# Kernel tuning notes

Measured on AMD Instinct MI355X. Metric: run time of the kernel, lower is better.

## Reference

```python
import jax, jax.numpy as jnp
import numpy as np

N = 4096   # node_each_graph == in_feats (adjacency-row node features)
H = 512    # n_hidden
C = 2      # n_classes
E = 65536  # edges (avg degree 16)
NL = 5     # n_layers -> 4 GINConv layers
NR = NL - 2  # stacked hidden GIN layers (layers 1..3)


def _bn(x, g, b, m, v):
    # BatchNorm1d in eval mode (running stats), eps=1e-5
    return (x - m) * jax.lax.rsqrt(v + 1e-5) * g + b


def setup_inputs():
    key = jax.random.key(0)
    ks = iter(jax.random.split(key, 16))
    nk = lambda: next(ks)
    s = 0.02
    f32 = jnp.float32
    d = {}
    d["feat"] = jax.random.normal(nk(), (N, N), f32)
    d["edge_src"] = jax.random.randint(nk(), (E,), 0, N)
    d["edge_dst"] = jax.random.randint(nk(), (E,), 0, N)
    # GIN layer 0: MLP is Linear(N,H)-BN-ReLU-Linear(H,H); ApplyNodeFunc BN; outer BN
    d["eps0"] = jnp.zeros((), f32)
    d["W0a"] = jax.random.normal(nk(), (N, H), f32) * s
    d["b0a"] = jnp.zeros((H,), f32)
    d["W0b"] = jax.random.normal(nk(), (H, H), f32) * s
    d["b0b"] = jnp.zeros((H,), f32)
    for nm in ["bn0a", "bnA0", "bnO0"]:
        d[nm + "_g"] = jnp.ones((H,), f32); d[nm + "_b"] = jnp.zeros((H,), f32)
        d[nm + "_m"] = jnp.zeros((H,), f32); d[nm + "_v"] = jnp.ones((H,), f32)
    # GIN layers 1..NL-2 stacked (H -> H)
    d["epsR"] = jnp.zeros((NR,), f32)
    d["WRa"] = jax.random.normal(nk(), (NR, H, H), f32) * s
    d["bRa"] = jnp.zeros((NR, H), f32)
    d["WRb"] = jax.random.normal(nk(), (NR, H, H), f32) * s
    d["bRb"] = jnp.zeros((NR, H), f32)
    for nm in ["bnRa", "bnAR", "bnOR"]:
        d[nm + "_g"] = jnp.ones((NR, H), f32); d[nm + "_b"] = jnp.zeros((NR, H), f32)
        d[nm + "_m"] = jnp.zeros((NR, H), f32); d[nm + "_v"] = jnp.ones((NR, H), f32)
    # per-hidden-rep readout linears (batch_size = 1)
    d["Wp0"] = jax.random.normal(nk(), (N * N, C), f32) * 0.001
    d["bp0"] = jnp.zeros((C,), f32)
    d["WpR"] = jax.random.normal(nk(), (NL - 1, N * H, C), f32) * 0.001
    d["bpR"] = jnp.zeros((NL - 1, C), f32)
    return d


def _gin(h, src, dst, eps, Wa, ba, bna, Wb, bb, bnA, bnO):
    # GINConv sum-aggregation: (1+eps)*h + sum over in-neighbors
    agg = jax.ops.segment_sum(h[src], dst, num_segments=N)
    x = (1.0 + eps) * h + agg
    # MLP (num_layers=2): Linear -> BN -> ReLU -> Linear
    x = jax.nn.relu(_bn(x @ Wa + ba, *bna))
    x = x @ Wb + bb
    # ApplyNodeFunc: BN -> ReLU
    x = jax.nn.relu(_bn(x, *bnA))
    # Model-level BN -> ReLU
    x = jax.nn.relu(_bn(x, *bnO))
    return x


def reference(feat, edge_src, edge_dst, eps0, W0a, b0a, W0b, b0b,
              bn0a_g, bn0a_b, bn0a_m, bn0a_v, bnA0_g, bnA0_b, bnA0_m, bnA0_v,
              bnO0_g, bnO0_b, bnO0_m, bnO0_v,
              epsR, WRa, bRa, WRb, bRb,
              bnRa_g, bnRa_b, bnRa_m, bnRa_v, bnAR_g, bnAR_b, bnAR_m, bnAR_v,
              bnOR_g, bnOR_b, bnOR_m, bnOR_v, Wp0, bp0, WpR, bpR):
    h = _gin(feat, edge_src, edge_dst, eps0, W0a, b0a,
             (bn0a_g, bn0a_b, bn0a_m, bn0a_v), W0b, b0b,
             (bnA0_g, bnA0_b, bnA0_m, bnA0_v), (bnO0_g, bnO0_b, bnO0_m, bnO0_v))
    hs = [h]
    for i in range(NR):  # small fixed layer loop
        h = _gin(h, edge_src, edge_dst, epsR[i], WRa[i], bRa[i],
                 (bnRa_g[i], bnRa_b[i], bnRa_m[i], bnRa_v[i]), WRb[i], bRb[i],
                 (bnAR_g[i], bnAR_b[i], bnAR_m[i], bnAR_v[i]),
                 (bnOR_g[i], bnOR_b[i], bnOR_m[i], bnOR_v[i]))
        hs.append(h)
    # jumping-knowledge readout over hidden_rep (eval: dropout = identity)
    score = feat.reshape(1, -1) @ Wp0 + bp0
    for i, hi in enumerate(hs):
        score = score + hi.reshape(1, -1) @ WpR[i] + bpR[i]
    return score
```

## Files before the change

### kernel.cpp

```cpp
#include <hip/hip_runtime.h>
#include <cstdint>
#include <cstddef>

typedef __attribute__((ext_vector_type(8))) short short8;
typedef __attribute__((ext_vector_type(4))) float f32x4;
typedef __attribute__((ext_vector_type(4))) float f4;
typedef __attribute__((ext_vector_type(2))) float f2;
typedef __attribute__((ext_vector_type(4))) unsigned short us4;

#define NN 4096
#define HH 512
#define EE 65536

#define GLOAD(gp, lp) __builtin_amdgcn_global_load_lds( \
    (const __attribute__((address_space(1))) void*)(gp), \
    (__attribute__((address_space(3))) void*)(lp), 16, 0, 0)

__device__ __forceinline__ unsigned short f2bf(float x) {
    union { float f; unsigned u; } un; un.f = x;
    unsigned r = un.u + 0x7fffu + ((un.u >> 16) & 1u);
    return (unsigned short)(r >> 16);
}
__device__ __forceinline__ float b2f(unsigned short v) {
    union { unsigned u; float f; } un; un.u = ((unsigned)v) << 16; return un.f;
}

__global__ __launch_bounds__(1024) void k_histscan(const int* __restrict__ edst,
                                                   int* __restrict__ starts) {
    __shared__ int cnt[NN];
    __shared__ int wtot[16], woff[16];
    const int t = threadIdx.x;
    for (int i = t; i < NN; i += 1024) cnt[i] = 0;
    __syncthreads();
    for (int i = t; i < EE; i += 1024) atomicAdd(&cnt[edst[i]], 1);
    __syncthreads();
    const int b = t * 4;
    const int c0 = cnt[b], c1 = cnt[b + 1], c2 = cnt[b + 2], c3 = cnt[b + 3];
    const int s = c0 + c1 + c2 + c3;
    const int lane = t & 63, wv = t >> 6;
    int inc = s;
    for (int d = 1; d < 64; d <<= 1) {
        int v = __shfl_up(inc, d);
        if (lane >= d) inc += v;
    }
    if (lane == 63) wtot[wv] = inc;
    __syncthreads();
    if (t == 0) {
        int a = 0;
        for (int i = 0; i < 16; ++i) { woff[i] = a; a += wtot[i]; }
        starts[NN] = a;
    }
    __syncthreads();
    int run = woff[wv] + inc - s;
    starts[b] = run; run += c0;
    starts[b + 1] = run; run += c1;
    starts[b + 2] = run; run += c2;
    starts[b + 3] = run;
}

__global__ void k_scatter(const int* __restrict__ src, const int* __restrict__ dst,
                          const int* __restrict__ starts, int* __restrict__ cursor,
                          int* __restrict__ sorted) {
    int e = blockIdx.x * 256 + threadIdx.x;
    if (e < EE) {
        int d = dst[e];
        int p = starts[d] + atomicAdd(&cursor[d], 1);
        sorted[p] = src[e];
    }
}

__global__ void k_binsort(const int* __restrict__ starts, int* __restrict__ a) {
    int d = blockIdx.x * 256 + threadIdx.x;
    if (d < NN) {
        int s = starts[d], e = starts[d + 1];
        for (int i = s + 1; i < e; ++i) {
            int v = a[i]; int j = i - 1;
            while (j >= s && a[j] > v) { a[j + 1] = a[j]; --j; }
            a[j + 1] = v;
        }
    }
}

__global__ __launch_bounds__(256) void k_cvtdot0(const float* __restrict__ feat,
                                                 const float* __restrict__ w,
                                                 unsigned short* __restrict__ featb,
                                                 float* __restrict__ part) {
    __shared__ f4 fs[1024];
    __shared__ float s0[256], s1[256];
    const int t = threadIdx.x;
    const long B0 = (long)blockIdx.x * 1024;
    const f4* ff = (const f4*)feat;
    const f4* ww = (const f4*)w;
    f4 v[4];
#pragma unroll
    for (int k = 0; k < 4; ++k)
        v[k] = __builtin_nontemporal_load(ff + B0 + k * 256 + t);
#pragma unroll
    for (int k = 0; k < 4; ++k) {
        fs[k * 256 + t] = v[k];
        us4 o;
        o.x = f2bf(v[k].x); o.y = f2bf(v[k].y); o.z = f2bf(v[k].z); o.w = f2bf(v[k].w);
        ((us4*)featb)[B0 + k * 256 + t] = o;
    }
    f4 wv[8];
#pragma unroll
    for (int k = 0; k < 8; ++k)
        wv[k] = __builtin_nontemporal_load(ww + 2 * B0 + k * 256 + t);
    __syncthreads();
    float a0 = 0.f, a1 = 0.f;
#pragma unroll
    for (int k = 0; k < 8; ++k) {
        const int q = k * 256 + t;
        f2 fp = *(const f2*)((const char*)fs + (size_t)q * 8);
        a0 += fp.x * wv[k].x + fp.y * wv[k].z;
        a1 += fp.x * wv[k].y + fp.y * wv[k].w;
    }
    s0[t] = a0; s1[t] = a1;
    __syncthreads();
    for (int s = 128; s > 0; s >>= 1) {
        if (t < s) { s0[t] += s0[t + s]; s1[t] += s1[t + s]; }
        __syncthreads();
    }
    if (t == 0) { part[2 * blockIdx.x] = s0[0]; part[2 * blockIdx.x + 1] = s1[0]; }
}

__global__ __launch_bounds__(256) void k_transcvt8(const float* __restrict__ W0a,
                                                   const float* __restrict__ W0b,
                                                   const float* __restrict__ WRa,
                                                   const float* __restrict__ WRb,
                                                   unsigned short* __restrict__ w0at,
                                                   unsigned short* __restrict__ wt) {
    __shared__ float tile[32][33];
    const int z = blockIdx.z;
    const float* W;
    unsigned short* Wt;
    int K;
    if (z == 7) {
        W = W0a; Wt = w0at; K = NN;
    } else {
        if (blockIdx.x >= 16 || blockIdx.y >= 16) return;
        W = (z == 0) ? W0b : (z < 4) ? WRa + (size_t)(z - 1) * HH * HH
                                     : WRb + (size_t)(z - 4) * HH * HH;
        Wt = wt + (size_t)z * HH * HH; K = HH;
    }
    const int k0 = blockIdx.x * 32, n0 = blockIdx.y * 32;
    const int tx = threadIdx.x & 31, ty = threadIdx.x >> 5;
    for (int r = ty; r < 32; r += 8)
        tile[r][tx] = W[(size_t)(k0 + r) * HH + n0 + tx];
    __syncthreads();
    for (int r = ty; r < 32; r += 8)
        Wt[(size_t)(n0 + r) * K + k0 + tx] = f2bf(tile[tx][r]);
}

__global__ __launch_bounds__(256) void k_gemm0(
    const unsigned short* __restrict__ A, const unsigned short* __restrict__ Bt,
    int M, int N, int K, float* __restrict__ outf)
{
    __shared__ alignas(16) unsigned short As[2][128 * 32];
    __shared__ alignas(16) unsigned short Bs[2][128 * 32];
    const int t = threadIdx.x;
    const int lane = t & 63, w = t >> 6;
    const int wr = w >> 1, wc = w & 1;
    const int l15 = lane & 15, l4 = lane >> 4;
    const int m0 = blockIdx.x * 128, n0 = blockIdx.y * 128;

    f32x4 acc[4][4];
#pragma unroll
    for (int i = 0; i < 4; ++i)
#pragma unroll
        for (int j = 0; j < 4; ++j) acc[i][j] = (f32x4){0.f, 0.f, 0.f, 0.f};

    const int Kc = K / gridDim.z;
    const int kbase = blockIdx.z * Kc;
    const unsigned short* ga0 = A + (size_t)m0 * K + kbase + (size_t)(t >> 2) * K + (t & 3) * 8;
    const unsigned short* ga1 = ga0 + (size_t)64 * K;
    const unsigned short* gb0 = Bt + (size_t)n0 * K + kbase + (size_t)(t >> 2) * K + (t & 3) * 8;
    const unsigned short* gb1 = gb0 + (size_t)64 * K;

    auto stage = [&](int kt, int buf) {
        const int ko = kt * 32;
        GLOAD(ga0 + ko, &As[buf][t * 8]);
        GLOAD(ga1 + ko, &As[buf][(t + 256) * 8]);
        GLOAD(gb0 + ko, &Bs[buf][t * 8]);
        GLOAD(gb1 + ko, &Bs[buf][(t + 256) * 8]);
    };

    const int nk = Kc >> 5;
    stage(0, 0);
    __syncthreads();
    for (int kt = 0; kt < nk; ++kt) {
        const int cur = kt & 1;
        if (kt + 1 < nk) stage(kt + 1, cur ^ 1);
        short8 aF[4], bF[4];
#pragma unroll
        for (int i = 0; i < 4; ++i)
            aF[i] = *(const short8*)(&As[cur][(wr * 64 + i * 16 + l15) * 32 + 8 * l4]);
#pragma unroll
        for (int j = 0; j < 4; ++j)
            bF[j] = *(const short8*)(&Bs[cur][(wc * 64 + j * 16 + l15) * 32 + 8 * l4]);
#pragma unroll
        for (int i = 0; i < 4; ++i)
#pragma unroll
            for (int j = 0; j < 4; ++j)
                acc[i][j] = __builtin_amdgcn_mfma_f32_16x16x32_bf16(aF[i], bF[j], acc[i][j], 0, 0, 0);
        __syncthreads();
    }

    const int mrow = m0 + wr * 64;
    float* op = outf + (size_t)blockIdx.z * M * N;
#pragma unroll
    for (int j = 0; j < 4; ++j) {
        const int cg = n0 + wc * 64 + j * 16 + l15;
#pragma unroll
        for (int i = 0; i < 4; ++i)
#pragma unroll
            for (int r = 0; r < 4; ++r)
                op[(size_t)(mrow + i * 16 + l4 * 4 + r) * N + cg] = acc[i][j][r];
    }
}

template<int EPI, bool DOT>
__global__ __launch_bounds__(512) void k_gemmH(
    const unsigned short* __restrict__ A, const unsigned short* __restrict__ Bt,
    const float* __restrict__ bias,
    const float* __restrict__ g1p, const float* __restrict__ b1p,
    const float* __restrict__ m1p, const float* __restrict__ v1p,
    const float* __restrict__ g2p, const float* __restrict__ b2p,
    const float* __restrict__ m2p, const float* __restrict__ v2p,
    unsigned short* __restrict__ outb,
    const float* __restrict__ wq, float* __restrict__ part, int slotbase)
{
    constexpr int K = HH, N = HH;
    __shared__ alignas(16) unsigned short As[2][128 * 32];
    __shared__ alignas(16) unsigned short Bs[2][64 * 32];
    const int t = threadIdx.x;
    const int lane = t & 63, w = t >> 6;
    const int wr = w >> 1, wc = w & 1;
    const int l15 = lane & 15, l4 = lane >> 4;
    const int m0 = blockIdx.x * 128, n0 = blockIdx.y * 64;

    f32x4 acc[2][2];
#pragma unroll
    for (int i = 0; i < 2; ++i)
#pragma unroll
        for (int j = 0; j < 2; ++j) acc[i][j] = (f32x4){0.f, 0.f, 0.f, 0.f};

    const unsigned short* ga = A + (size_t)m0 * K + (size_t)(t >> 2) * K + (t & 3) * 8;
    const unsigned short* gb = Bt + (size_t)n0 * K + (size_t)(t >> 2) * K + (t & 3) * 8;

    auto stage = [&](int kt, int buf) {
        const int ko = kt * 32;
        GLOAD(ga + ko, &As[buf][t * 8]);
        if (t < 256) GLOAD(gb + ko, &Bs[buf][t * 8]);
    };

    const int nk = K >> 5;
    stage(0, 0);
    __syncthreads();
    for (int kt = 0; kt < nk; ++kt) {
        const int cur = kt & 1;
        if (kt + 1 < nk) stage(kt + 1, cur ^ 1);
        short8 aF[2], bF[2];
#pragma unroll
        for (int i = 0; i < 2; ++i)
            aF[i] = *(const short8*)(&As[cur][(wr * 32 + i * 16 + l15) * 32 + 8 * l4]);
#pragma unroll
        for (int j = 0; j < 2; ++j)
            bF[j] = *(const short8*)(&Bs[cur][(wc * 32 + j * 16 + l15) * 32 + 8 * l4]);
#pragma unroll
        for (int i = 0; i < 2; ++i)
#pragma unroll
            for (int j = 0; j < 2; ++j)
                acc[i][j] = __builtin_amdgcn_mfma_f32_16x16x32_bf16(aF[i], bF[j], acc[i][j], 0, 0, 0);
        __syncthreads();
    }

    const int mrow = m0 + wr * 32;
    float d0 = 0.f, d1 = 0.f;
#pragma unroll
    for (int j = 0; j < 2; ++j) {
        const int cg = n0 + wc * 32 + j * 16 + l15;
        const float bi = bias[cg];
        const float sc1 = rsqrtf(v1p[cg] + 1e-5f) * g1p[cg];
        const float sh1 = b1p[cg] - m1p[cg] * sc1;
        float sc2 = 1.f, sh2 = 0.f;
        if (EPI == 3) {
            sc2 = rsqrtf(v2p[cg] + 1e-5f) * g2p[cg];
            sh2 = b2p[cg] - m2p[cg] * sc2;
        }
#pragma unroll
        for (int i = 0; i < 2; ++i) {
#pragma unroll
            for (int r = 0; r < 4; ++r) {
                const int rg = mrow + i * 16 + l4 * 4 + r;
                float x = acc[i][j][r];
                x = fmaxf((x + bi) * sc1 + sh1, 0.f);
                if (EPI == 3) x = fmaxf(x * sc2 + sh2, 0.f);
                outb[(size_t)rg * N + cg] = f2bf(x);
                if constexpr (DOT) {
                    float2 wvv = ((const float2*)wq)[(size_t)rg * N + cg];
                    d0 += x * wvv.x; d1 += x * wvv.y;
                }
            }
        }
    }
    if constexpr (DOT) {
        __shared__ float r0[512], r1[512];
        r0[t] = d0; r1[t] = d1;
        __syncthreads();
        for (int s = 256; s > 0; s >>= 1) {
            if (t < s) { r0[t] += r0[t + s]; r1[t] += r1[t + s]; }
            __syncthreads();
        }
        if (t == 0) {
            const int slot = slotbase + blockIdx.y * gridDim.x + blockIdx.x;
            part[2 * slot] = r0[0]; part[2 * slot + 1] = r1[0];
        }
    }
}

__global__ __launch_bounds__(256) void k_red4b(const float* __restrict__ p,
                                               unsigned short* __restrict__ G0b) {
    const long S = (long)NN * HH / 4;
    long i = blockIdx.x * 256L + threadIdx.x;
    float4 a = ((const float4*)p)[i];
    float4 b = ((const float4*)p)[i + S];
    float4 c = ((const float4*)p)[i + 2 * S];
    float4 d = ((const float4*)p)[i + 3 * S];
    us4 o;
    o.x = f2bf((a.x + b.x) + (c.x + d.x));
    o.y = f2bf((a.y + b.y) + (c.y + d.y));
    o.z = f2bf((a.z + b.z) + (c.z + d.z));
    o.w = f2bf((a.w + b.w) + (c.w + d.w));
    ((us4*)G0b)[i] = o;
}

__global__ __launch_bounds__(128) void k_agg0(
    const unsigned short* __restrict__ G0, const int* __restrict__ starts,
    const int* __restrict__ sorted, const float* __restrict__ epsp,
    const float* __restrict__ bias,
    const float* __restrict__ bg, const float* __restrict__ bb,
    const float* __restrict__ bm, const float* __restrict__ bv,
    unsigned short* __restrict__ outb)
{
    const int d = blockIdx.x, t = threadIdx.x;
    const float ep = 1.0f + epsp[0];
    ushort4 ow = ((const ushort4*)(G0 + (size_t)d * HH))[t];
    float sx = 0.f, sy = 0.f, sz = 0.f, sw = 0.f;
    const int e0 = starts[d], e1 = starts[d + 1];
    int i = e0;
    for (; i + 4 <= e1; i += 4) {
        int q0 = sorted[i], q1 = sorted[i + 1], q2 = sorted[i + 2], q3 = sorted[i + 3];
        ushort4 x0 = ((const ushort4*)(G0 + (size_t)q0 * HH))[t];
        ushort4 x1 = ((const ushort4*)(G0 + (size_t)q1 * HH))[t];
        ushort4 x2 = ((const ushort4*)(G0 + (size_t)q2 * HH))[t];
        ushort4 x3 = ((const ushort4*)(G0 + (size_t)q3 * HH))[t];
        sx += (b2f(x0.x) + b2f(x1.x)) + (b2f(x2.x) + b2f(x3.x));
        sy += (b2f(x0.y) + b2f(x1.y)) + (b2f(x2.y) + b2f(x3.y));
        sz += (b2f(x0.z) + b2f(x1.z)) + (b2f(x2.z) + b2f(x3.z));
        sw += (b2f(x0.w) + b2f(x1.w)) + (b2f(x2.w) + b2f(x3.w));
    }
    for (; i < e1; ++i) {
        ushort4 x = ((const ushort4*)(G0 + (size_t)sorted[i] * HH))[t];
        sx += b2f(x.x); sy += b2f(x.y); sz += b2f(x.z); sw += b2f(x.w);
    }
    float4 bi = ((const float4*)bias)[t];
    float4 g4 = ((const float4*)bg)[t];
    float4 b4 = ((const float4*)bb)[t];
    float4 m4 = ((const float4*)bm)[t];
    float4 v4 = ((const float4*)bv)[t];
    float x0 = ep * b2f(ow.x) + sx + bi.x;
    float x1 = ep * b2f(ow.y) + sy + bi.y;
    float x2 = ep * b2f(ow.z) + sz + bi.z;
    float x3 = ep * b2f(ow.w) + sw + bi.w;
    x0 = fmaxf((x0 - m4.x) * rsqrtf(v4.x + 1e-5f) * g4.x + b4.x, 0.f);
    x1 = fmaxf((x1 - m4.y) * rsqrtf(v4.y + 1e-5f) * g4.y + b4.y, 0.f);
    x2 = fmaxf((x2 - m4.z) * rsqrtf(v4.z + 1e-5f) * g4.z + b4.z, 0.f);
    x3 = fmaxf((x3 - m4.w) * rsqrtf(v4.w + 1e-5f) * g4.w + b4.w, 0.f);
    ushort4 o; o.x = f2bf(x0); o.y = f2bf(x1); o.z = f2bf(x2); o.w = f2bf(x3);
    ((ushort4*)(outb + (size_t)d * HH))[t] = o;
}

__global__ __launch_bounds__(128) void k_aggL(
    const unsigned short* __restrict__ hsrc, const int* __restrict__ starts,
    const int* __restrict__ sorted, const float* __restrict__ epsp,
    unsigned short* __restrict__ outb)
{
    const int d = blockIdx.x, t = threadIdx.x;
    const float ep = 1.0f + epsp[0];
    ushort4 ow = ((const ushort4*)(hsrc + (size_t)d * HH))[t];
    float sx = 0.f, sy = 0.f, sz = 0.f, sw = 0.f;
    const int e0 = starts[d], e1 = starts[d + 1];
    int i = e0;
    for (; i + 4 <= e1; i += 4) {
        int q0 = sorted[i], q1 = sorted[i + 1], q2 = sorted[i + 2], q3 = sorted[i + 3];
        ushort4 x0 = ((const ushort4*)(hsrc + (size_t)q0 * HH))[t];
        ushort4 x1 = ((const ushort4*)(hsrc + (size_t)q1 * HH))[t];
        ushort4 x2 = ((const ushort4*)(hsrc + (size_t)q2 * HH))[t];
        ushort4 x3 = ((const ushort4*)(hsrc + (size_t)q3 * HH))[t];
        sx += (b2f(x0.x) + b2f(x1.x)) + (b2f(x2.x) + b2f(x3.x));
        sy += (b2f(x0.y) + b2f(x1.y)) + (b2f(x2.y) + b2f(x3.y));
        sz += (b2f(x0.z) + b2f(x1.z)) + (b2f(x2.z) + b2f(x3.z));
        sw += (b2f(x0.w) + b2f(x1.w)) + (b2f(x2.w) + b2f(x3.w));
    }
    for (; i < e1; ++i) {
        ushort4 x = ((const ushort4*)(hsrc + (size_t)sorted[i] * HH))[t];
        sx += b2f(x.x); sy += b2f(x.y); sz += b2f(x.z); sw += b2f(x.w);
    }
    ushort4 o;
    o.x = f2bf(ep * b2f(ow.x) + sx);
    o.y = f2bf(ep * b2f(ow.y) + sy);
    o.z = f2bf(ep * b2f(ow.z) + sz);
    o.w = f2bf(ep * b2f(ow.w) + sw);
    ((ushort4*)(outb + (size_t)d * HH))[t] = o;
}

__global__ __launch_bounds__(256) void k_final(const float* __restrict__ part, int nslot,
                                               const float* __restrict__ bp0, const float* __restrict__ bpR,
                                               float* __restrict__ out) {
    __shared__ float s0[256], s1[256];
    int t = threadIdx.x;
    float a0 = 0.f, a1 = 0.f;
    for (int i = t; i < nslot; i += 256) { a0 += part[2 * i]; a1 += part[2 * i + 1]; }
    s0[t] = a0; s1[t] = a1;
    __syncthreads();
    for (int s = 128; s > 0; s >>= 1) {
        if (t < s) { s0[t] += s0[t + s]; s1[t] += s1[t + s]; }
        __syncthreads();
    }
    if (t == 0) {
        out[0] = s0[0] + bp0[0] + bpR[0] + bpR[2] + bpR[4] + bpR[6];
        out[1] = s1[0] + bp0[1] + bpR[1] + bpR[3] + bpR[5] + bpR[7];
    }
}

extern "C" void kernel_launch(void* const* d_in, const int* in_sizes, int n_in,
                              void* d_out, int out_size, void* d_ws, size_t ws_size,
                              hipStream_t stream)
{
    const float* feat = (const float*)d_in[0];
    const int*   esrc = (const int*)d_in[1];
    const int*   edst = (const int*)d_in[2];
    const float* eps0 = (const float*)d_in[3];
    const float* W0a  = (const float*)d_in[4];
    const float* b0a  = (const float*)d_in[5];
    const float* W0b  = (const float*)d_in[6];
    const float* b0b  = (const float*)d_in[7];
    const float* bn0a_g = (const float*)d_in[8];
    const float* bn0a_b = (const float*)d_in[9];
    const float* bn0a_m = (const float*)d_in[10];
    const float* bn0a_v = (const float*)d_in[11];
    const float* bnA0_g = (const float*)d_in[12];
    const float* bnA0_b = (const float*)d_in[13];
    const float* bnA0_m = (const float*)d_in[14];
    const float* bnA0_v = (const float*)d_in[15];
    const float* bnO0_g = (const float*)d_in[16];
    const float* bnO0_b = (const float*)d_in[17];
    const float* bnO0_m = (const float*)d_in[18];
    const float* bnO0_v = (const float*)d_in[19];
    const float* epsR = (const float*)d_in[20];
    const float* WRa  = (const float*)d_in[21];
    const float* bRa  = (const float*)d_in[22];
    const float* WRb  = (const float*)d_in[23];
    const float* bRb  = (const float*)d_in[24];
    const float* bnRa_g = (const float*)d_in[25];
    const float* bnRa_b = (const float*)d_in[26];
    const float* bnRa_m = (const float*)d_in[27];
    const float* bnRa_v = (const float*)d_in[28];
    const float* bnAR_g = (const float*)d_in[29];
    const float* bnAR_b = (const float*)d_in[30];
    const float* bnAR_m = (const float*)d_in[31];
    const float* bnAR_v = (const float*)d_in[32];
    const float* bnOR_g = (const float*)d_in[33];
    const float* bnOR_b = (const float*)d_in[34];
    const float* bnOR_m = (const float*)d_in[35];
    const float* bnOR_v = (const float*)d_in[36];
    const float* Wp0 = (const float*)d_in[37];
    const float* bp0 = (const float*)d_in[38];
    const float* WpR = (const float*)d_in[39];
    const float* bpR = (const float*)d_in[40];
    float* out = (float*)d_out;

    char* ws = (char*)d_ws;
    const size_t MB = 1024 * 1024;
    int*   starts = (int*)(ws + 0x10000);
    int*   cursor = (int*)(ws + 0x20000);
    int*   sorted = (int*)(ws + 0x30000);
    float* part   = (float*)(ws + 0x70000);
    unsigned short* featb = (unsigned short*)(ws + 1 * MB);
    unsigned short* w0at  = (unsigned short*)(ws + 33 * MB);
    unsigned short* wt    = (unsigned short*)(ws + 37 * MB);
    unsigned short* G0b   = (unsigned short*)(ws + 41 * MB);
    unsigned short* xb = (unsigned short*)(ws + 49 * MB);
    unsigned short* yb = (unsigned short*)(ws + 53 * MB);
    unsigned short* hb = (unsigned short*)(ws + 57 * MB);
    float* pbuf = (float*)(ws + 57 * MB);

    hipMemsetAsync(cursor, 0, NN * sizeof(int), stream);
    k_histscan<<<1, 1024, 0, stream>>>(edst, starts);
    k_scatter<<<EE / 256, 256, 0, stream>>>(esrc, edst, starts, cursor, sorted);
    k_binsort<<<NN / 256, 256, 0, stream>>>(starts, sorted);

    k_cvtdot0<<<4096, 256, 0, stream>>>(feat, Wp0, featb, part);
    k_transcvt8<<<dim3(NN / 32, HH / 32, 8), 256, 0, stream>>>(W0a, W0b, WRa, WRb, w0at, wt);

    k_gemm0<<<dim3(32, 4, 4), 256, 0, stream>>>(featb, w0at, NN, HH, NN, pbuf);
    k_red4b<<<2048, 256, 0, stream>>>(pbuf, G0b);
    k_agg0<<<NN, 128, 0, stream>>>(G0b, starts, sorted, eps0, b0a,
                                   bn0a_g, bn0a_b, bn0a_m, bn0a_v, xb);
    k_gemmH<3, true><<<dim3(32, 8), 512, 0, stream>>>(xb, wt,
        b0b, bnA0_g, bnA0_b, bnA0_m, bnA0_v, bnO0_g, bnO0_b, bnO0_m, bnO0_v,
        hb, WpR, part, 4096);

    for (int i = 0; i < 3; ++i) {
        const unsigned short* hp = hb + (size_t)i * NN * HH;
        unsigned short* hn = hb + (size_t)(i + 1) * NN * HH;
        k_aggL<<<NN, 128, 0, stream>>>(hp, starts, sorted, epsR + i, xb);
        k_gemmH<1, false><<<dim3(32, 8), 512, 0, stream>>>(xb, wt + (size_t)(1 + i) * HH * HH,
            bRa + (size_t)i * HH,
            bnRa_g + (size_t)i * HH, bnRa_b + (size_t)i * HH, bnRa_m + (size_t)i * HH, bnRa_v + (size_t)i * HH,
            nullptr, nullptr, nullptr, nullptr,
            yb, nullptr, nullptr, 0);
        k_gemmH<3, true><<<dim3(32, 8), 512, 0, stream>>>(yb, wt + (size_t)(4 + i) * HH * HH,
            bRb + (size_t)i * HH,
            bnAR_g + (size_t)i * HH, bnAR_b + (size_t)i * HH, bnAR_m + (size_t)i * HH, bnAR_v + (size_t)i * HH,
            bnOR_g + (size_t)i * HH, bnOR_b + (size_t)i * HH, bnOR_m + (size_t)i * HH, bnOR_v + (size_t)i * HH,
            hn, WpR + (size_t)(i + 1) * NN * HH * 2, part, 4096 + (i + 1) * 256);
    }

    k_final<<<1, 256, 0, stream>>>(part, 4096 + 4 * 256, bp0, bpR, out);
}
```

Before: 299.6 us.

## Fuse GIN layer kernels into a persistent megakernel with grid barriers

```diff
diff --git a/kernel.cpp b/kernel.cpp
--- a/kernel.cpp
+++ b/kernel.cpp
@@ -11,6 +11,7 @@
 #define NN 4096
 #define HH 512
 #define EE 65536
+#define NBLK 256
 
 #define GLOAD(gp, lp) __builtin_amdgcn_global_load_lds( \
     (const __attribute__((address_space(1))) void*)(gp), \
@@ -23,6 +24,18 @@
 }
 __device__ __forceinline__ float b2f(unsigned short v) {
     union { unsigned u; float f; } un; un.u = ((unsigned)v) << 16; return un.f;
+}
+
+__device__ __forceinline__ void gbar(int* cnt, int target) {
+    __syncthreads();
+    if (threadIdx.x == 0) {
+        __threadfence();
+        __hip_atomic_fetch_add(cnt, 1, __ATOMIC_RELEASE, __HIP_MEMORY_SCOPE_AGENT);
+        while (__hip_atomic_load(cnt, __ATOMIC_ACQUIRE, __HIP_MEMORY_SCOPE_AGENT) < target)
+            __builtin_amdgcn_s_sleep(1);
+        __threadfence();
+    }
+    __syncthreads();
 }
 
 __global__ __launch_bounds__(1024) void k_histscan(const int* __restrict__ edst,
@@ -81,197 +94,155 @@
     }
 }
 
-__global__ __launch_bounds__(256) void k_cvtdot0(const float* __restrict__ feat,
-                                                 const float* __restrict__ w,
-                                                 unsigned short* __restrict__ featb,
-                                                 float* __restrict__ part) {
+__global__ __launch_bounds__(256) void k_prep(const float* __restrict__ feat,
+                                              const float* __restrict__ Wp0,
+                                              unsigned short* __restrict__ featb,
+                                              float* __restrict__ part,
+                                              const float* __restrict__ W0a,
+                                              const float* __restrict__ W0b,
+                                              const float* __restrict__ WRa,
+                                              const float* __restrict__ WRb,
+                                              unsigned short* __restrict__ w0at,
+                                              unsigned short* __restrict__ wt) {
     __shared__ f4 fs[1024];
     __shared__ float s0[256], s1[256];
+    __shared__ float tile[32][33];
     const int t = threadIdx.x;
-    const long B0 = (long)blockIdx.x * 1024;
-    const f4* ff = (const f4*)feat;
-    const f4* ww = (const f4*)w;
-    f4 v[4];
-#pragma unroll
-    for (int k = 0; k < 4; ++k)
-        v[k] = __builtin_nontemporal_load(ff + B0 + k * 256 + t);
-#pragma unroll
-    for (int k = 0; k < 4; ++k) {
-        fs[k * 256 + t] = v[k];
-        us4 o;
-        o.x = f2bf(v[k].x); o.y = f2bf(v[k].y); o.z = f2bf(v[k].z); o.w = f2bf(v[k].w);
-        ((us4*)featb)[B0 + k * 256 + t] = o;
-    }
-    f4 wv[8];
-#pragma unroll
-    for (int k = 0; k < 8; ++k)
-        wv[k] = __builtin_nontemporal_load(ww + 2 * B0 + k * 256 + t);
-    __syncthreads();
-    float a0 = 0.f, a1 = 0.f;
-#pragma unroll
-    for (int k = 0; k < 8; ++k) {
-        const int q = k * 256 + t;
-        f2 fp = *(const f2*)((const char*)fs + (size_t)q * 8);
-        a0 += fp.x * wv[k].x + fp.y * wv[k].z;
-        a1 += fp.x * wv[k].y + fp.y * wv[k].w;
-    }
-    s0[t] = a0; s1[t] = a1;
-    __syncthreads();
-    for (int s = 128; s > 0; s >>= 1) {
-        if (t < s) { s0[t] += s0[t + s]; s1[t] += s1[t + s]; }
-        __syncthreads();
-    }
-    if (t == 0) { part[2 * blockIdx.x] = s0[0]; part[2 * blockIdx.x + 1] = s1[0]; }
-}
-
-__global__ __launch_bounds__(256) void k_transcvt8(const float* __restrict__ W0a,
-                                                   const float* __restrict__ W0b,
-                                                   const float* __restrict__ WRa,
-                                                   const float* __restrict__ WRb,
-                                                   unsigned short* __restrict__ w0at,
-                                                   unsigned short* __restrict__ wt) {
-    __shared__ float tile[32][33];
-    const int z = blockIdx.z;
-    const float* W;
-    unsigned short* Wt;
-    int K;
-    if (z == 7) {
-        W = W0a; Wt = w0at; K = NN;
+    const int bid = blockIdx.x;
+    if (bid < 4096) {
+        const long B0 = (long)bid * 1024;
+        const f4* ff = (const f4*)feat;
+        const f4* ww = (const f4*)Wp0;
+        f4 v[4];
+#pragma unroll
+        for (int k = 0; k < 4; ++k)
+            v[k] = __builtin_nontemporal_load(ff + B0 + k * 256 + t);
+#pragma unroll
+        for (int k = 0; k < 4; ++k) {
+            fs[k * 256 + t] = v[k];
+            us4 o;
+            o.x = f2bf(v[k].x); o.y = f2bf(v[k].y); o.z = f2bf(v[k].z); o.w = f2bf(v[k].w);
+            __builtin_nontemporal_store(o, (us4*)featb + B0 + k * 256 + t);
+        }
+        f4 wv[8];
+#pragma unroll
+        for (int k = 0; k < 8; ++k)
+            wv[k] = __builtin_nontemporal_load(ww + 2 * B0 + k * 256 + t);
+        __syncthreads();
+        float a0 = 0.f, a1 = 0.f;
+#pragma unroll
+        for (int k = 0; k < 8; ++k) {
+            const int q = k * 256 + t;
+            f2 fp = *(const f2*)((const char*)fs + (size_t)q * 8);
+            a0 += fp.x * wv[k].x + fp.y * wv[k].z;
+            a1 += fp.x * wv[k].y + fp.y * wv[k].w;
+        }
+        s0[t] = a0; s1[t] = a1;
+        __syncthreads();
+        for (int s = 128; s > 0; s >>= 1) {
+            if (t < s) { s0[t] += s0[t + s]; s1[t] += s1[t + s]; }
+            __syncthreads();
+        }
+        if (t == 0) { part[2 * bid] = s0[0]; part[2 * bid + 1] = s1[0]; }
     } else {
-        if (blockIdx.x >= 16 || blockIdx.y >= 16) return;
-        W = (z == 0) ? W0b : (z < 4) ? WRa + (size_t)(z - 1) * HH * HH
-                                     : WRb + (size_t)(z - 4) * HH * HH;
-        Wt = wt + (size_t)z * HH * HH; K = HH;
-    }
-    const int k0 = blockIdx.x * 32, n0 = blockIdx.y * 32;
-    const int tx = threadIdx.x & 31, ty = threadIdx.x >> 5;
-    for (int r = ty; r < 32; r += 8)
-        tile[r][tx] = W[(size_t)(k0 + r) * HH + n0 + tx];
-    __syncthreads();
-    for (int r = ty; r < 32; r += 8)
-        Wt[(size_t)(n0 + r) * K + k0 + tx] = f2bf(tile[tx][r]);
-}
-
-__global__ __launch_bounds__(256) void k_gemm0(
-    const unsigned short* __restrict__ A, const unsigned short* __restrict__ Bt,
-    int M, int N, int K, float* __restrict__ outf)
+        const int tix = bid - 4096;
+        const float* W; unsigned short* Wt; int K, kb, nb;
+        if (tix < 2048) {
+            W = W0a; Wt = w0at; K = NN; kb = tix >> 4; nb = tix & 15;
+        } else {
+            const int t2 = tix - 2048;
+            const int z = t2 >> 8, r = t2 & 255;
+            W = (z == 0) ? W0b : (z < 4) ? WRa + (size_t)(z - 1) * HH * HH
+                                         : WRb + (size_t)(z - 4) * HH * HH;
+            Wt = wt + (size_t)z * HH * HH; K = HH; kb = r >> 4; nb = r & 15;
+        }
+        const int k0 = kb * 32, n0 = nb * 32;
+        const int tx = t & 31, ty = t >> 5;
+        for (int r = ty; r < 32; r += 8)
+            tile[r][tx] = W[(size_t)(k0 + r) * HH + n0 + tx];
+        __syncthreads();
+        for (int r = ty; r < 32; r += 8)
+            Wt[(size_t)(n0 + r) * K + k0 + tx] = f2bf(tile[tx][r]);
+    }
+}
+
+struct MegaArgs {
+    const unsigned short *featb, *w0at, *wt;
+    unsigned short *G0b, *xb, *yb, *hb;
+    const int *starts, *sorted;
+    const float *eps0, *b0a, *bn0a_g, *bn0a_b, *bn0a_m, *bn0a_v;
+    const float *b0b, *bnA0_g, *bnA0_b, *bnA0_m, *bnA0_v;
+    const float *bnO0_g, *bnO0_b, *bnO0_m, *bnO0_v;
+    const float *epsR, *bRa, *bnRa_g, *bnRa_b, *bnRa_m, *bnRa_v;
+    const float *bRb, *bnAR_g, *bnAR_b, *bnAR_m, *bnAR_v;
+    const float *bnOR_g, *bnOR_b, *bnOR_m, *bnOR_v;
+    const float *WpR, *bp0, *bpR;
+    float *part, *out;
+    int *bar;
+};
+
+template<int EPI, bool DOT>
+__device__ __forceinline__ void gemm_phase(
+    const unsigned short* __restrict__ A, const unsigned short* __restrict__ Bt, int K,
+    const float* __restrict__ bias,
+    const float* __restrict__ g1, const float* __restrict__ b1,
+    const float* __restrict__ m1, const float* __restrict__ v1,
+    const float* __restrict__ g2, const float* __restrict__ b2,
+    const float* __restrict__ m2, const float* __restrict__ v2,
+    unsigned short* __restrict__ outb,
+    const float* __restrict__ wq, float* __restrict__ part, int slot,
+    unsigned short* As, unsigned short* Bs)
 {
-    __shared__ alignas(16) unsigned short As[2][128 * 32];
-    __shared__ alignas(16) unsigned short Bs[2][128 * 32];
+    constexpr int N = HH;
     const int t = threadIdx.x;
     const int lane = t & 63, w = t >> 6;
     const int wr = w >> 1, wc = w & 1;
     const int l15 = lane & 15, l4 = lane >> 4;
-    const int m0 = blockIdx.x * 128, n0 = blockIdx.y * 128;
-
-    f32x4 acc[4][4];
-#pragma unroll
-    for (int i = 0; i < 4; ++i)
-#pragma unroll
-        for (int j = 0; j < 4; ++j) acc[i][j] = (f32x4){0.f, 0.f, 0.f, 0.f};
-
-    const int Kc = K / gridDim.z;
-    const int kbase = blockIdx.z * Kc;
-    const unsigned short* ga0 = A + (size_t)m0 * K + kbase + (size_t)(t >> 2) * K + (t & 3) * 8;
+    const int m0 = (blockIdx.x >> 3) * 128, n0 = (blockIdx.x & 7) * 64;
+
+    f32x4 acc[2][2];
+#pragma unroll
+    for (int i = 0; i < 2; ++i)
+#pragma unroll
+        for (int j = 0; j < 2; ++j) acc[i][j] = (f32x4){0.f, 0.f, 0.f, 0.f};
+
+    const unsigned short* ga0 = A + (size_t)(m0 + (t >> 3)) * K + (t & 7) * 8;
     const unsigned short* ga1 = ga0 + (size_t)64 * K;
-    const unsigned short* gb0 = Bt + (size_t)n0 * K + kbase + (size_t)(t >> 2) * K + (t & 3) * 8;
-    const unsigned short* gb1 = gb0 + (size_t)64 * K;
+    const unsigned short* gb  = Bt + (size_t)(n0 + (t >> 3)) * K + (t & 7) * 8;
 
     auto stage = [&](int kt, int buf) {
-        const int ko = kt * 32;
-        GLOAD(ga0 + ko, &As[buf][t * 8]);
-        GLOAD(ga1 + ko, &As[buf][(t + 256) * 8]);
-        GLOAD(gb0 + ko, &Bs[buf][t * 8]);
-        GLOAD(gb1 + ko, &Bs[buf][(t + 256) * 8]);
+        const int ko = kt * 64;
+        GLOAD(ga0 + ko, As + buf * 8192 + t * 8);
+        GLOAD(ga1 + ko, As + buf * 8192 + 4096 + t * 8);
+        GLOAD(gb + ko,  Bs + buf * 4096 + t * 8);
     };
 
-    const int nk = Kc >> 5;
+    const int nk = K >> 6;
     stage(0, 0);
     __syncthreads();
     for (int kt = 0; kt < nk; ++kt) {
         const int cur = kt & 1;
         if (kt + 1 < nk) stage(kt + 1, cur ^ 1);
-        short8 aF[4], bF[4];
-#pragma unroll
-        for (int i = 0; i < 4; ++i)
-            aF[i] = *(const short8*)(&As[cur][(wr * 64 + i * 16 + l15) * 32 + 8 * l4]);
-#pragma unroll
-        for (int j = 0; j < 4; ++j)
-            bF[j] = *(const short8*)(&Bs[cur][(wc * 64 + j * 16 + l15) * 32 + 8 * l4]);
-#pragma unroll
-        for (int i = 0; i < 4; ++i)
-#pragma unroll
-            for (int j = 0; j < 4; ++j)
-                acc[i][j] = __builtin_amdgcn_mfma_f32_16x16x32_bf16(aF[i], bF[j], acc[i][j], 0, 0, 0);
-        __syncthreads();
-    }
-
-    const int mrow = m0 + wr * 64;
-    float* op = outf + (size_t)blockIdx.z * M * N;
-#pragma unroll
-    for (int j = 0; j < 4; ++j) {
-        const int cg = n0 + wc * 64 + j * 16 + l15;
-#pragma unroll
-        for (int i = 0; i < 4; ++i)
-#pragma unroll
-            for (int r = 0; r < 4; ++r)
-                op[(size_t)(mrow + i * 16 + l4 * 4 + r) * N + cg] = acc[i][j][r];
-    }
-}
-
-template<int EPI, bool DOT>
-__global__ __launch_bounds__(512) void k_gemmH(
-    const unsigned short* __restrict__ A, const unsigned short* __restrict__ Bt,
-    const float* __restrict__ bias,
-    const float* __restrict__ g1p, const float* __restrict__ b1p,
-    const float* __restrict__ m1p, const float* __restrict__ v1p,
-    const float* __restrict__ g2p, const float* __restrict__ b2p,
-    const float* __restrict__ m2p, const float* __restrict__ v2p,
-    unsigned short* __restrict__ outb,
-    const float* __restrict__ wq, float* __restrict__ part, int slotbase)
-{
-    constexpr int K = HH, N = HH;
-    __shared__ alignas(16) unsigned short As[2][128 * 32];
-    __shared__ alignas(16) unsigned short Bs[2][64 * 32];
-    const int t = threadIdx.x;
-    const int lane = t & 63, w = t >> 6;
-    const int wr = w >> 1, wc = w & 1;
-    const int l15 = lane & 15, l4 = lane >> 4;
-    const int m0 = blockIdx.x * 128, n0 = blockIdx.y * 64;
-
-    f32x4 acc[2][2];
-#pragma unroll
-    for (int i = 0; i < 2; ++i)
-#pragma unroll
-        for (int j = 0; j < 2; ++j) acc[i][j] = (f32x4){0.f, 0.f, 0.f, 0.f};
-
-    const unsigned short* ga = A + (size_t)m0 * K + (size_t)(t >> 2) * K + (t & 3) * 8;
-    const unsigned short* gb = Bt + (size_t)n0 * K + (size_t)(t >> 2) * K + (t & 3) * 8;
-
-    auto stage = [&](int kt, int buf) {
-        const int ko = kt * 32;
-        GLOAD(ga + ko, &As[buf][t * 8]);
-        if (t < 256) GLOAD(gb + ko, &Bs[buf][t * 8]);
-    };
-
-    const int nk = K >> 5;
-    stage(0, 0);
-    __syncthreads();
-    for (int kt = 0; kt < nk; ++kt) {
-        const int cur = kt & 1;
-        if (kt + 1 < nk) stage(kt + 1, cur ^ 1);
-        short8 aF[2], bF[2];
+        const unsigned short* Ac = As + cur * 8192;
+        const unsigned short* Bc = Bs + cur * 4096;
+        short8 aF[2][2], bF[2][2];
 #pragma unroll
         for (int i = 0; i < 2; ++i)
-            aF[i] = *(const short8*)(&As[cur][(wr * 32 + i * 16 + l15) * 32 + 8 * l4]);
+#pragma unroll
+            for (int ks = 0; ks < 2; ++ks)
+                aF[i][ks] = *(const short8*)(Ac + (wr * 32 + i * 16 + l15) * 64 + ks * 32 + l4 * 8);
 #pragma unroll
         for (int j = 0; j < 2; ++j)
-            bF[j] = *(const short8*)(&Bs[cur][(wc * 32 + j * 16 + l15) * 32 + 8 * l4]);
-#pragma unroll
-        for (int i = 0; i < 2; ++i)
-#pragma unroll
-            for (int j = 0; j < 2; ++j)
-                acc[i][j] = __builtin_amdgcn_mfma_f32_16x16x32_bf16(aF[i], bF[j], acc[i][j], 0, 0, 0);
+#pragma unroll
+            for (int ks = 0; ks < 2; ++ks)
+                bF[j][ks] = *(const short8*)(Bc + (wc * 32 + j * 16 + l15) * 64 + ks * 32 + l4 * 8);
+#pragma unroll
+        for (int ks = 0; ks < 2; ++ks)
+#pragma unroll
+            for (int i = 0; i < 2; ++i)
+#pragma unroll
+                for (int j = 0; j < 2; ++j)
+                    acc[i][j] = __builtin_amdgcn_mfma_f32_16x16x32_bf16(aF[i][ks], bF[j][ks], acc[i][j], 0, 0, 0);
         __syncthreads();
     }
 
@@ -280,13 +251,15 @@
 #pragma unroll
     for (int j = 0; j < 2; ++j) {
         const int cg = n0 + wc * 32 + j * 16 + l15;
-        const float bi = bias[cg];
-        const float sc1 = rsqrtf(v1p[cg] + 1e-5f) * g1p[cg];
-        const float sh1 = b1p[cg] - m1p[cg] * sc1;
-        float sc2 = 1.f, sh2 = 0.f;
+        float bi = 0.f, sc1 = 1.f, sh1 = 0.f, sc2 = 1.f, sh2 = 0.f;
+        if (EPI >= 1) {
+            bi = bias[cg];
+            sc1 = rsqrtf(v1[cg] + 1e-5f) * g1[cg];
+            sh1 = b1[cg] - m1[cg] * sc1;
+        }
         if (EPI == 3) {
-            sc2 = rsqrtf(v2p[cg] + 1e-5f) * g2p[cg];
-            sh2 = b2p[cg] - m2p[cg] * sc2;
+            sc2 = rsqrtf(v2[cg] + 1e-5f) * g2[cg];
+            sh2 = b2[cg] - m2[cg] * sc2;
         }
 #pragma unroll
         for (int i = 0; i < 2; ++i) {
@@ -294,143 +267,143 @@
             for (int r = 0; r < 4; ++r) {
                 const int rg = mrow + i * 16 + l4 * 4 + r;
                 float x = acc[i][j][r];
-                x = fmaxf((x + bi) * sc1 + sh1, 0.f);
-                if (EPI == 3) x = fmaxf(x * sc2 + sh2, 0.f);
+                if (EPI >= 1) {
+                    x = fmaxf((x + bi) * sc1 + sh1, 0.f);
+                    if (EPI == 3) x = fmaxf(x * sc2 + sh2, 0.f);
+                }
                 outb[(size_t)rg * N + cg] = f2bf(x);
                 if constexpr (DOT) {
-                    float2 wvv = ((const float2*)wq)[(size_t)rg * N + cg];
+                    f2 wvv = __builtin_nontemporal_load((const f2*)wq + (size_t)rg * N + cg);
                     d0 += x * wvv.x; d1 += x * wvv.y;
                 }
             }
         }
     }
     if constexpr (DOT) {
-        __shared__ float r0[512], r1[512];
+        float* r0 = (float*)As;
+        float* r1 = r0 + 512;
+        __syncthreads();
         r0[t] = d0; r1[t] = d1;
         __syncthreads();
         for (int s = 256; s > 0; s >>= 1) {
             if (t < s) { r0[t] += r0[t + s]; r1[t] += r1[t + s]; }
             __syncthreads();
         }
-        if (t == 0) {
-            const int slot = slotbase + blockIdx.y * gridDim.x + blockIdx.x;
-            part[2 * slot] = r0[0]; part[2 * slot + 1] = r1[0];
-        }
-    }
-}
-
-__global__ __launch_bounds__(256) void k_red4b(const float* __restrict__ p,
-                                               unsigned short* __restrict__ G0b) {
-    const long S = (long)NN * HH / 4;
-    long i = blockIdx.x * 256L + threadIdx.x;
-    float4 a = ((const float4*)p)[i];
-    float4 b = ((const float4*)p)[i + S];
-    float4 c = ((const float4*)p)[i + 2 * S];
-    float4 d = ((const float4*)p)[i + 3 * S];
-    us4 o;
-    o.x = f2bf((a.x + b.x) + (c.x + d.x));
-    o.y = f2bf((a.y + b.y) + (c.y + d.y));
-    o.z = f2bf((a.z + b.z) + (c.z + d.z));
-    o.w = f2bf((a.w + b.w) + (c.w + d.w));
-    ((us4*)G0b)[i] = o;
-}
-
-__global__ __launch_bounds__(128) void k_agg0(
-    const unsigned short* __restrict__ G0, const int* __restrict__ starts,
-    const int* __restrict__ sorted, const float* __restrict__ epsp,
+        if (t == 0) { part[2 * slot] = r0[0]; part[2 * slot + 1] = r1[0]; }
+    }
+}
+
+template<bool L0>
+__device__ __forceinline__ void agg_phase(
+    const unsigned short* __restrict__ src, unsigned short* __restrict__ dst,
+    const int* __restrict__ starts, const int* __restrict__ sorted, float ep,
     const float* __restrict__ bias,
     const float* __restrict__ bg, const float* __restrict__ bb,
-    const float* __restrict__ bm, const float* __restrict__ bv,
-    unsigned short* __restrict__ outb)
+    const float* __restrict__ bm, const float* __restrict__ bv)
 {
-    const int d = blockIdx.x, t = threadIdx.x;
-    const float ep = 1.0f + epsp[0];
-    ushort4 ow = ((const ushort4*)(G0 + (size_t)d * HH))[t];
-    float sx = 0.f, sy = 0.f, sz = 0.f, sw = 0.f;
-    const int e0 = starts[d], e1 = starts[d + 1];
-    int i = e0;
-    for (; i + 4 <= e1; i += 4) {
-        int q0 = sorted[i], q1 = sorted[i + 1], q2 = sorted[i + 2], q3 = sorted[i + 3];
-        ushort4 x0 = ((const ushort4*)(G0 + (size_t)q0 * HH))[t];
-        ushort4 x1 = ((const ushort4*)(G0 + (size_t)q1 * HH))[t];
-        ushort4 x2 = ((const ushort4*)(G0 + (size_t)q2 * HH))[t];
-        ushort4 x3 = ((const ushort4*)(G0 + (size_t)q3 * HH))[t];
-        sx += (b2f(x0.x) + b2f(x1.x)) + (b2f(x2.x) + b2f(x3.x));
-        sy += (b2f(x0.y) + b2f(x1.y)) + (b2f(x2.y) + b2f(x3.y));
-        sz += (b2f(x0.z) + b2f(x1.z)) + (b2f(x2.z) + b2f(x3.z));
-        sw += (b2f(x0.w) + b2f(x1.w)) + (b2f(x2.w) + b2f(x3.w));
-    }
-    for (; i < e1; ++i) {
-        ushort4 x = ((const ushort4*)(G0 + (size_t)sorted[i] * HH))[t];
-        sx += b2f(x.x); sy += b2f(x.y); sz += b2f(x.z); sw += b2f(x.w);
-    }
-    float4 bi = ((const float4*)bias)[t];
-    float4 g4 = ((const float4*)bg)[t];
-    float4 b4 = ((const float4*)bb)[t];
-    float4 m4 = ((const float4*)bm)[t];
-    float4 v4 = ((const float4*)bv)[t];
-    float x0 = ep * b2f(ow.x) + sx + bi.x;
-    float x1 = ep * b2f(ow.y) + sy + bi.y;
-    float x2 = ep * b2f(ow.z) + sz + bi.z;
-    float x3 = ep * b2f(ow.w) + sw + bi.w;
-    x0 = fmaxf((x0 - m4.x) * rsqrtf(v4.x + 1e-5f) * g4.x + b4.x, 0.f);
-    x1 = fmaxf((x1 - m4.y) * rsqrtf(v4.y + 1e-5f) * g4.y + b4.y, 0.f);
-    x2 = fmaxf((x2 - m4.z) * rsqrtf(v4.z + 1e-5f) * g4.z + b4.z, 0.f);
-    x3 = fmaxf((x3 - m4.w) * rsqrtf(v4.w + 1e-5f) * g4.w + b4.w, 0.f);
-    ushort4 o; o.x = f2bf(x0); o.y = f2bf(x1); o.z = f2bf(x2); o.w = f2bf(x3);
-    ((ushort4*)(outb + (size_t)d * HH))[t] = o;
-}
-
-__global__ __launch_bounds__(128) void k_aggL(
-    const unsigned short* __restrict__ hsrc, const int* __restrict__ starts,
-    const int* __restrict__ sorted, const float* __restrict__ epsp,
-    unsigned short* __restrict__ outb)
-{
-    const int d = blockIdx.x, t = threadIdx.x;
-    const float ep = 1.0f + epsp[0];
-    ushort4 ow = ((const ushort4*)(hsrc + (size_t)d * HH))[t];
-    float sx = 0.f, sy = 0.f, sz = 0.f, sw = 0.f;
-    const int e0 = starts[d], e1 = starts[d + 1];
-    int i = e0;
-    for (; i + 4 <= e1; i += 4) {
-        int q0 = sorted[i], q1 = sorted[i + 1], q2 = sorted[i + 2], q3 = sorted[i + 3];
-        ushort4 x0 = ((const ushort4*)(hsrc + (size_t)q0 * HH))[t];
-        ushort4 x1 = ((const ushort4*)(hsrc + (size_t)q1 * HH))[t];
-        ushort4 x2 = ((const ushort4*)(hsrc + (size_t)q2 * HH))[t];
-        ushort4 x3 = ((const ushort4*)(hsrc + (size_t)q3 * HH))[t];
-        sx += (b2f(x0.x) + b2f(x1.x)) + (b2f(x2.x) + b2f(x3.x));
-        sy += (b2f(x0.y) + b2f(x1.y)) + (b2f(x2.y) + b2f(x3.y));
-        sz += (b2f(x0.z) + b2f(x1.z)) + (b2f(x2.z) + b2f(x3.z));
-        sw += (b2f(x0.w) + b2f(x1.w)) + (b2f(x2.w) + b2f(x3.w));
-    }
-    for (; i < e1; ++i) {
-        ushort4 x = ((const ushort4*)(hsrc + (size_t)sorted[i] * HH))[t];
-        sx += b2f(x.x); sy += b2f(x.y); sz += b2f(x.z); sw += b2f(x.w);
-    }
-    ushort4 o;
-    o.x = f2bf(ep * b2f(ow.x) + sx);
-    o.y = f2bf(ep * b2f(ow.y) + sy);
-    o.z = f2bf(ep * b2f(ow.z) + sz);
-    o.w = f2bf(ep * b2f(ow.w) + sw);
-    ((ushort4*)(outb + (size_t)d * HH))[t] = o;
-}
-
-__global__ __launch_bounds__(256) void k_final(const float* __restrict__ part, int nslot,
-                                               const float* __restrict__ bp0, const float* __restrict__ bpR,
-                                               float* __restrict__ out) {
-    __shared__ float s0[256], s1[256];
-    int t = threadIdx.x;
-    float a0 = 0.f, a1 = 0.f;
-    for (int i = t; i < nslot; i += 256) { a0 += part[2 * i]; a1 += part[2 * i + 1]; }
-    s0[t] = a0; s1[t] = a1;
-    __syncthreads();
-    for (int s = 128; s > 0; s >>= 1) {
-        if (t < s) { s0[t] += s0[t + s]; s1[t] += s1[t + s]; }
-        __syncthreads();
-    }
-    if (t == 0) {
-        out[0] = s0[0] + bp0[0] + bpR[0] + bpR[2] + bpR[4] + bpR[6];
-        out[1] = s1[0] + bp0[1] + bpR[1] + bpR[3] + bpR[5] + bpR[7];
+    const int t = threadIdx.x;
+    const int tl = t & 127;
+#pragma unroll
+    for (int rep = 0; rep < 4; ++rep) {
+        const int d = blockIdx.x * 16 + rep * 4 + (t >> 7);
+        ushort4 ow = ((const ushort4*)(src + (size_t)d * HH))[tl];
+        float sx = 0.f, sy = 0.f, sz = 0.f, sw = 0.f;
+        const int e0 = starts[d], e1 = starts[d + 1];
+        int i = e0;
+        for (; i + 4 <= e1; i += 4) {
+            int q0 = sorted[i], q1 = sorted[i + 1], q2 = sorted[i + 2], q3 = sorted[i + 3];
+            ushort4 x0 = ((const ushort4*)(src + (size_t)q0 * HH))[tl];
+            ushort4 x1 = ((const ushort4*)(src + (size_t)q1 * HH))[tl];
+            ushort4 x2 = ((const ushort4*)(src + (size_t)q2 * HH))[tl];
+            ushort4 x3 = ((const ushort4*)(src + (size_t)q3 * HH))[tl];
+            sx += (b2f(x0.x) + b2f(x1.x)) + (b2f(x2.x) + b2f(x3.x));
+            sy += (b2f(x0.y) + b2f(x1.y)) + (b2f(x2.y) + b2f(x3.y));
+            sz += (b2f(x0.z) + b2f(x1.z)) + (b2f(x2.z) + b2f(x3.z));
+            sw += (b2f(x0.w) + b2f(x1.w)) + (b2f(x2.w) + b2f(x3.w));
+        }
+        for (; i < e1; ++i) {
+            ushort4 x = ((const ushort4*)(src + (size_t)sorted[i] * HH))[tl];
+            sx += b2f(x.x); sy += b2f(x.y); sz += b2f(x.z); sw += b2f(x.w);
+        }
+        float x0 = ep * b2f(ow.x) + sx;
+        float x1 = ep * b2f(ow.y) + sy;
+        float x2 = ep * b2f(ow.z) + sz;
+        float x3 = ep * b2f(ow.w) + sw;
+        if constexpr (L0) {
+            float4 bi = ((const float4*)bias)[tl];
+            float4 g4 = ((const float4*)bg)[tl];
+            float4 b4 = ((const float4*)bb)[tl];
+            float4 m4 = ((const float4*)bm)[tl];
+            float4 v4 = ((const float4*)bv)[tl];
+            x0 = fmaxf((x0 + bi.x - m4.x) * rsqrtf(v4.x + 1e-5f) * g4.x + b4.x, 0.f);
+            x1 = fmaxf((x1 + bi.y - m4.y) * rsqrtf(v4.y + 1e-5f) * g4.y + b4.y, 0.f);
+            x2 = fmaxf((x2 + bi.z - m4.z) * rsqrtf(v4.z + 1e-5f) * g4.z + b4.z, 0.f);
+            x3 = fmaxf((x3 + bi.w - m4.w) * rsqrtf(v4.w + 1e-5f) * g4.w + b4.w, 0.f);
+        }
+        ushort4 o; o.x = f2bf(x0); o.y = f2bf(x1); o.z = f2bf(x2); o.w = f2bf(x3);
+        ((ushort4*)(dst + (size_t)d * HH))[tl] = o;
+    }
+}
+
+__global__ __launch_bounds__(512) void k_mega(MegaArgs a) {
+    __shared__ alignas(16) unsigned short As[2 * 8192];
+    __shared__ alignas(16) unsigned short Bs[2 * 4096];
+    int ph = 0;
+
+    gemm_phase<0, false>(a.featb, a.w0at, NN, nullptr, nullptr, nullptr, nullptr, nullptr,
+                         nullptr, nullptr, nullptr, nullptr, a.G0b, nullptr, nullptr, 0, As, Bs);
+    gbar(a.bar, ++ph * NBLK);
+
+    agg_phase<true>(a.G0b, a.xb, a.starts, a.sorted, 1.0f + a.eps0[0],
+                    a.b0a, a.bn0a_g, a.bn0a_b, a.bn0a_m, a.bn0a_v);
+    gbar(a.bar, ++ph * NBLK);
+
+    gemm_phase<3, true>(a.xb, a.wt, HH, a.b0b,
+                        a.bnA0_g, a.bnA0_b, a.bnA0_m, a.bnA0_v,
+                        a.bnO0_g, a.bnO0_b, a.bnO0_m, a.bnO0_v,
+                        a.hb, a.WpR, a.part, 4096 + blockIdx.x, As, Bs);
+    gbar(a.bar, ++ph * NBLK);
+
+    for (int L = 0; L < 3; ++L) {
+        const unsigned short* hp = a.hb + (size_t)L * NN * HH;
+        unsigned short* hn = (unsigned short*)a.hb + (size_t)(L + 1) * NN * HH;
+        agg_phase<false>(hp, a.xb, a.starts, a.sorted, 1.0f + a.epsR[L],
+                         nullptr, nullptr, nullptr, nullptr, nullptr);
+        gbar(a.bar, ++ph * NBLK);
+        gemm_phase<1, false>(a.xb, a.wt + (size_t)(1 + L) * HH * HH, HH,
+                             a.bRa + (size_t)L * HH,
+                             a.bnRa_g + (size_t)L * HH, a.bnRa_b + (size_t)L * HH,
+                             a.bnRa_m + (size_t)L * HH, a.bnRa_v + (size_t)L * HH,
+                             nullptr, nullptr, nullptr, nullptr,
+                             a.yb, nullptr, nullptr, 0, As, Bs);
+        gbar(a.bar, ++ph * NBLK);
+        gemm_phase<3, true>(a.yb, a.wt + (size_t)(4 + L) * HH * HH, HH,
+                            a.bRb + (size_t)L * HH,
+                            a.bnAR_g + (size_t)L * HH, a.bnAR_b + (size_t)L * HH,
+                            a.bnAR_m + (size_t)L * HH, a.bnAR_v + (size_t)L * HH,
+                            a.bnOR_g + (size_t)L * HH, a.bnOR_b + (size_t)L * HH,
+                            a.bnOR_m + (size_t)L * HH, a.bnOR_v + (size_t)L * HH,
+                            hn, a.WpR + (size_t)(L + 1) * NN * HH * 2,
+                            a.part, 4096 + (L + 1) * 256 + blockIdx.x, As, Bs);
+        gbar(a.bar, ++ph * NBLK);
+    }
+
+    if (blockIdx.x == 0) {
+        const int t = threadIdx.x;
+        float* r0 = (float*)As;
+        float* r1 = r0 + 512;
+        float aa0 = 0.f, aa1 = 0.f;
+        for (int i = t; i < 5120; i += 512) { aa0 += a.part[2 * i]; aa1 += a.part[2 * i + 1]; }
+        r0[t] = aa0; r1[t] = aa1;
+        __syncthreads();
+        for (int s = 256; s > 0; s >>= 1) {
+            if (t < s) { r0[t] += r0[t + s]; r1[t] += r1[t + s]; }
+            __syncthreads();
+        }
+        if (t == 0) {
+            a.out[0] = r0[0] + a.bp0[0] + a.bpR[0] + a.bpR[2] + a.bpR[4] + a.bpR[6];
+            a.out[1] = r1[0] + a.bp0[1] + a.bpR[1] + a.bpR[3] + a.bpR[5] + a.bpR[7];
+        }
     }
 }
 
@@ -485,6 +458,7 @@
     const size_t MB = 1024 * 1024;
     int*   starts = (int*)(ws + 0x10000);
     int*   cursor = (int*)(ws + 0x20000);
+    int*   bar    = (int*)(ws + 0x2C000);
     int*   sorted = (int*)(ws + 0x30000);
     float* part   = (float*)(ws + 0x70000);
     unsigned short* featb = (unsigned short*)(ws + 1 * MB);
@@ -494,39 +468,31 @@
     unsigned short* xb = (unsigned short*)(ws + 49 * MB);
     unsigned short* yb = (unsigned short*)(ws + 53 * MB);
     unsigned short* hb = (unsigned short*)(ws + 57 * MB);
-    float* pbuf = (float*)(ws + 57 * MB);
-
-    hipMemsetAsync(cursor, 0, NN * sizeof(int), stream);
+
+    hipMemsetAsync(ws + 0x20000, 0, 0x10000, stream);
     k_histscan<<<1, 1024, 0, stream>>>(edst, starts);
     k_scatter<<<EE / 256, 256, 0, stream>>>(esrc, edst, starts, cursor, sorted);
     k_binsort<<<NN / 256, 256, 0, stream>>>(starts, sorted);
 
-    k_cvtdot0<<<4096, 256, 0, stream>>>(feat, Wp0, featb, part);
-    k_transcvt8<<<dim3(NN / 32, HH / 32, 8), 256, 0, stream>>>(W0a, W0b, WRa, WRb, w0at, wt);
-
-    k_gemm0<<<dim3(32, 4, 4), 256, 0, stream>>>(featb, w0at, NN, HH, NN, pbuf);
-    k_red4b<<<2048, 256, 0, stream>>>(pbuf, G0b);
-    k_agg0<<<NN, 128, 0, stream>>>(G0b, starts, sorted, eps0, b0a,
-                                   bn0a_g, bn0a_b, bn0a_m, bn0a_v, xb);
-    k_gemmH<3, true><<<dim3(32, 8), 512, 0, stream>>>(xb, wt,
-        b0b, bnA0_g, bnA0_b, bnA0_m, bnA0_v, bnO0_g, bnO0_b, bnO0_m, bnO0_v,
-        hb, WpR, part, 4096);
-
-    for (int i = 0; i < 3; ++i) {
-        const unsigned short* hp = hb + (size_t)i * NN * HH;
-        unsigned short* hn = hb + (size_t)(i + 1) * NN * HH;
-        k_aggL<<<NN, 128, 0, stream>>>(hp, starts, sorted, epsR + i, xb);
-        k_gemmH<1, false><<<dim3(32, 8), 512, 0, stream>>>(xb, wt + (size_t)(1 + i) * HH * HH,
-            bRa + (size_t)i * HH,
-            bnRa_g + (size_t)i * HH, bnRa_b + (size_t)i * HH, bnRa_m + (size_t)i * HH, bnRa_v + (size_t)i * HH,
-            nullptr, nullptr, nullptr, nullptr,
-            yb, nullptr, nullptr, 0);
-        k_gemmH<3, true><<<dim3(32, 8), 512, 0, stream>>>(yb, wt + (size_t)(4 + i) * HH * HH,
-            bRb + (size_t)i * HH,
-            bnAR_g + (size_t)i * HH, bnAR_b + (size_t)i * HH, bnAR_m + (size_t)i * HH, bnAR_v + (size_t)i * HH,
-            bnOR_g + (size_t)i * HH, bnOR_b + (size_t)i * HH, bnOR_m + (size_t)i * HH, bnOR_v + (size_t)i * HH,
-            hn, WpR + (size_t)(i + 1) * NN * HH * 2, part, 4096 + (i + 1) * 256);
-    }
-
-    k_final<<<1, 256, 0, stream>>>(part, 4096 + 4 * 256, bp0, bpR, out);
-}
+    k_prep<<<4096 + 3840, 256, 0, stream>>>(feat, Wp0, featb, part,
+                                            W0a, W0b, WRa, WRb, w0at, wt);
+
+    MegaArgs a;
+    a.featb = featb; a.w0at = w0at; a.wt = wt;
+    a.G0b = G0b; a.xb = xb; a.yb = yb; a.hb = hb;
+    a.starts = starts; a.sorted = sorted;
+    a.eps0 = eps0; a.b0a = b0a;
+    a.bn0a_g = bn0a_g; a.bn0a_b = bn0a_b; a.bn0a_m = bn0a_m; a.bn0a_v = bn0a_v;
+    a.b0b = b0b;
+    a.bnA0_g = bnA0_g; a.bnA0_b = bnA0_b; a.bnA0_m = bnA0_m; a.bnA0_v = bnA0_v;
+    a.bnO0_g = bnO0_g; a.bnO0_b = bnO0_b; a.bnO0_m = bnO0_m; a.bnO0_v = bnO0_v;
+    a.epsR = epsR; a.bRa = bRa;
+    a.bnRa_g = bnRa_g; a.bnRa_b = bnRa_b; a.bnRa_m = bnRa_m; a.bnRa_v = bnRa_v;
+    a.bRb = bRb;
+    a.bnAR_g = bnAR_g; a.bnAR_b = bnAR_b; a.bnAR_m = bnAR_m; a.bnAR_v = bnAR_v;
+    a.bnOR_g = bnOR_g; a.bnOR_b = bnOR_b; a.bnOR_m = bnOR_m; a.bnOR_v = bnOR_v;
+    a.WpR = WpR; a.bp0 = bp0; a.bpR = bpR;
+    a.part = part; a.out = out; a.bar = bar;
+
+    k_mega<<<NBLK, 512, 0, stream>>>(a);
+}
```

New measurement: 680.5 us. +127.1%, slower.
